# Kernel tuning notes

Hardware: AMD Instinct MI355X
Metric: run time of the kernel (lower is better)

Reference implementation:

```python
import jax, jax.numpy as jnp
import numpy as np

H = 1024   # hidden size
NH = 16    # num attention heads
HD = H // NH  # head dim = 64


def setup_inputs() -> dict:
    key = jax.random.key(0)
    ks = jax.random.split(key, 8)
    B, S = 2, 2048
    scale = 0.02
    return {
        "hidden_states": jax.random.normal(ks[0], (B, S, H), dtype=jnp.float32),
        "attention_mask": jnp.zeros((B, 1, 1, S), dtype=jnp.float32),
        "Wq": jax.random.normal(ks[1], (H, H), dtype=jnp.float32) * scale,
        "bq": jnp.zeros((H,), dtype=jnp.float32),
        "Wk": jax.random.normal(ks[2], (H, H), dtype=jnp.float32) * scale,
        "bk": jnp.zeros((H,), dtype=jnp.float32),
        "Wv": jax.random.normal(ks[3], (H, H), dtype=jnp.float32) * scale,
        "bv": jnp.zeros((H,), dtype=jnp.float32),
    }


def reference(hidden_states, attention_mask, Wq, bq, Wk, bk, Wv, bv):
    B, S, _ = hidden_states.shape

    def split_heads(x):  # [B,S,H] -> [B,NH,S,HD]
        return x.reshape(B, S, NH, HD).transpose(0, 2, 1, 3)

    q = split_heads(hidden_states @ Wq.T + bq)
    k = split_heads(hidden_states @ Wk.T + bk)
    v = split_heads(hidden_states @ Wv.T + bv)

    # raw attention scores [B,NH,S,S]
    scores = jnp.einsum("bhqd,bhkd->bhqk", q, k) / jnp.sqrt(jnp.float32(HD))
    scores = scores + attention_mask  # additive mask, broadcast [B,1,1,S]
    probs = jax.nn.softmax(scores, axis=-1)
    # dropout(p=0.1) is identity in eval mode

    ctx = jnp.einsum("bhqk,bhkd->bhqd", probs, v)  # [B,NH,S,HD]
    return ctx.transpose(0, 2, 1, 3).reshape(B, S, H)
```

## Files before the change

kernel.cpp:

```cpp
#include <hip/hip_runtime.h>
#include <hip/hip_bf16.h>
#include <math.h>

#define HSZ 1024
#define NHD 16
#define SEQ 2048
#define BSZ 2
#define MTOT (BSZ*SEQ)

typedef __attribute__((ext_vector_type(4)))  float  f32x4;
typedef __attribute__((ext_vector_type(8)))  __bf16 bf16x8;

#define LOG2E 1.4426950408889634f

#if __has_builtin(__builtin_amdgcn_exp2f)
#define EXP2(x) __builtin_amdgcn_exp2f(x)
#else
#define EXP2(x) exp2f(x)
#endif

__device__ __forceinline__ unsigned short f2bf(float x) {
    union { float f; unsigned u; } v; v.f = x;
    unsigned r = v.u + 0x7FFFu + ((v.u >> 16) & 1u);
    return (unsigned short)(r >> 16);
}
__device__ __forceinline__ float bf2f(unsigned short u) {
    union { unsigned u; float f; } v; v.u = ((unsigned)u) << 16; return v.f;
}
__device__ __forceinline__ unsigned cvtpk(float lo, float hi) {
    unsigned r;
    asm("v_cvt_pk_bf16_f32 %0, %1, %2" : "=v"(r) : "v"(lo), "v"(hi));
    return r;
}

__global__ __launch_bounds__(256) void cvt_all(
    const float* __restrict__ h,  unsigned short* __restrict__ hd,
    const float* __restrict__ w0, unsigned short* __restrict__ w0d,
    const float* __restrict__ w1, unsigned short* __restrict__ w1d,
    const float* __restrict__ w2, unsigned short* __restrict__ w2d,
    const float* __restrict__ mask, unsigned short* __restrict__ mexpb)
{
    const int bid = blockIdx.x;
    if (bid >= 3584) {
        const int o = ((bid - 3584) * 256 + threadIdx.x) * 8;
        float4 a = *(const float4*)(mask + o);
        float4 b = *(const float4*)(mask + o + 4);
        uint4 v;
        v.x = f2bf(EXP2(a.x * LOG2E)) | ((unsigned)f2bf(EXP2(a.y * LOG2E)) << 16);
        v.y = f2bf(EXP2(a.z * LOG2E)) | ((unsigned)f2bf(EXP2(a.w * LOG2E)) << 16);
        v.z = f2bf(EXP2(b.x * LOG2E)) | ((unsigned)f2bf(EXP2(b.y * LOG2E)) << 16);
        v.w = f2bf(EXP2(b.z * LOG2E)) | ((unsigned)f2bf(EXP2(b.w * LOG2E)) << 16);
        *(uint4*)(mexpb + o) = v;
        return;
    }
    const float* s; unsigned short* d; int i;
    if (bid < 2048)      { s = h;  d = hd;  i = bid; }
    else if (bid < 2560) { s = w0; d = w0d; i = bid - 2048; }
    else if (bid < 3072) { s = w1; d = w1d; i = bid - 2560; }
    else                 { s = w2; d = w2d; i = bid - 3072; }
    const int o = (i * 256 + threadIdx.x) * 8;
    float4 a = *(const float4*)(s + o);
    float4 b = *(const float4*)(s + o + 4);
    uint4 v;
    v.x = f2bf(a.x) | ((unsigned)f2bf(a.y) << 16);
    v.y = f2bf(a.z) | ((unsigned)f2bf(a.w) << 16);
    v.z = f2bf(b.x) | ((unsigned)f2bf(b.y) << 16);
    v.w = f2bf(b.z) | ((unsigned)f2bf(b.w) << 16);
    *(uint4*)(d + o) = v;
}

__global__ __launch_bounds__(256) void qkv_gemm(
    const unsigned short* __restrict__ hb,
    const unsigned short* __restrict__ wq,
    const unsigned short* __restrict__ wk,
    const unsigned short* __restrict__ wv,
    const float* __restrict__ bq, const float* __restrict__ bk,
    const float* __restrict__ bv, const unsigned short* __restrict__ mexpb,
    unsigned short* __restrict__ qo, char* __restrict__ ko,
    char* __restrict__ vo)
{
    __shared__ __align__(16) unsigned short As[128 * 32];
    __shared__ __align__(16) unsigned short Bs[128 * 32];

    const int t = threadIdx.x;
    const int w = t >> 6, l = t & 63, g = l >> 4, c = l & 15;
    const int bn = blockIdx.x, bm = blockIdx.y;
    const int which = bn >> 3;
    const int n0 = (bn & 7) << 7;
    const int m0 = bm << 7;
    const unsigned short* W = (which == 0) ? wq : (which == 1) ? wk : wv;
    const float* bb = (which == 0) ? bq : (which == 1) ? bk : bv;
    const float scale = (which == 0) ? 0.125f * LOG2E : 1.0f;
    const int wr = w >> 1, wc = w & 1;

    float mexpf[16];
    if (which == 2) {
        #pragma unroll
        for (int mi = 0; mi < 4; ++mi) {
            const int mrow = m0 + wr * 64 + mi * 16 + g * 4;
            const int bi = mrow >> 11, si = mrow & 2047;
            const unsigned short* mp = mexpb + bi * SEQ + si;
            uint2 mv = *(const uint2*)mp;
            mexpf[mi * 4 + 0] = bf2f((unsigned short)(mv.x & 0xFFFF));
            mexpf[mi * 4 + 1] = bf2f((unsigned short)(mv.x >> 16));
            mexpf[mi * 4 + 2] = bf2f((unsigned short)(mv.y & 0xFFFF));
            mexpf[mi * 4 + 3] = bf2f((unsigned short)(mv.y >> 16));
        }
    }

    f32x4 acc[4][4];
    #pragma unroll
    for (int mi = 0; mi < 4; ++mi)
        #pragma unroll
        for (int ni = 0; ni < 4; ++ni) acc[mi][ni] = {0.f, 0.f, 0.f, 0.f};

    for (int k0 = 0; k0 < HSZ; k0 += 32) {
        #pragma unroll
        for (int i2 = 0; i2 < 2; ++i2) {
            const int chunk = 2 * w + i2;
            const int row = (chunk << 4) + (l >> 2);
            const int sg = (l & 3) ^ ((row >> 1) & 3);
            const char* ga = (const char*)hb +
                (((size_t)(m0 + row) << 10) + k0) * 2 + sg * 16;
            const char* gb = (const char*)W +
                (((size_t)(n0 + row) << 10) + k0) * 2 + sg * 16;
            __builtin_amdgcn_global_load_lds(
                (const __attribute__((address_space(1))) unsigned*)ga,
                (__attribute__((address_space(3))) unsigned*)((char*)As + chunk * 1024),
                16, 0, 0);
            __builtin_amdgcn_global_load_lds(
                (const __attribute__((address_space(1))) unsigned*)gb,
                (__attribute__((address_space(3))) unsigned*)((char*)Bs + chunk * 1024),
                16, 0, 0);
        }
        __syncthreads();

        bf16x8 af[4], bfr[4];
        #pragma unroll
        for (int mi = 0; mi < 4; ++mi) {
            const int row = wr * 64 + mi * 16 + c;
            const int gg = g ^ ((row >> 1) & 3);
            af[mi] = *(const bf16x8*)((const char*)As + row * 64 + gg * 16);
        }
        #pragma unroll
        for (int ni = 0; ni < 4; ++ni) {
            const int row = wc * 64 + ni * 16 + c;
            const int gg = g ^ ((row >> 1) & 3);
            bfr[ni] = *(const bf16x8*)((const char*)Bs + row * 64 + gg * 16);
        }
        #pragma unroll
        for (int mi = 0; mi < 4; ++mi)
            #pragma unroll
            for (int ni = 0; ni < 4; ++ni)
                acc[mi][ni] = __builtin_amdgcn_mfma_f32_16x16x32_bf16(
                    af[mi], bfr[ni], acc[mi][ni], 0, 0, 0);
        __syncthreads();
    }

    #pragma unroll
    for (int ni = 0; ni < 4; ++ni) {
        const int ncol = n0 + wc * 64 + ni * 16 + c;
        const int hh = ncol >> 6, d = ncol & 63;
        const float bsc = bb[ncol] * scale;
        #pragma unroll
        for (int mi = 0; mi < 4; ++mi) {
            #pragma unroll
            for (int j = 0; j < 4; ++j) {
                const int mrow = m0 + wr * 64 + mi * 16 + g * 4 + j;
                const int bi = mrow >> 11, si = mrow & 2047;
                float vf = acc[mi][ni][j] * scale + bsc;
                if (which == 2) vf *= mexpf[mi * 4 + j];
                const unsigned short val = f2bf(vf);
                const size_t bhoff = (size_t)(bi * NHD + hh);
                if (which == 0) {
                    qo[((bhoff * SEQ + si) << 6) + d] = val;
                } else if (which == 1) {
                    char* p = ko + (bhoff << 18) + ((size_t)(si >> 6) << 13)
                            + ((si & 63) << 7) + (((d << 1)) ^ ((si & 7) << 4));
                    *(unsigned short*)p = val;
                } else {
                    char* p = vo + (bhoff << 18) + ((size_t)(si >> 6) << 13)
                            + (d << 7) + (((si & 63) << 1) ^ ((d & 7) << 4));
                    *(unsigned short*)p = val;
                }
            }
        }
    }
}

__global__ __launch_bounds__(256) void attn_mfma(
    const unsigned short* __restrict__ qb, const char* __restrict__ kb,
    const char* __restrict__ vb, const unsigned short* __restrict__ mexpb,
    float* __restrict__ out)
{
    __shared__ __align__(16) char Kt[2][8192];
    __shared__ __align__(16) char Vt[2][8192];
    __shared__ __align__(16) unsigned Pl[4][16][32];

    const int t = threadIdx.x;
    const int w = t >> 6, l = t & 63, g = l >> 4, c = l & 15;
    const int qt = blockIdx.x, h = blockIdx.y, b = blockIdx.z;
    const int bh = b * NHD + h;
    const int q0 = qt * 64 + w * 16;

    const unsigned short* qp = qb + ((size_t)bh * SEQ + q0) * 64;
    const char* kbase = kb + ((size_t)bh << 18);
    const char* vbase = vb + ((size_t)bh << 18);
    const unsigned short* mep = mexpb + b * SEQ;

    bf16x8 qf[2];
    #pragma unroll
    for (int p = 0; p < 2; ++p)
        qf[p] = *(const bf16x8*)(qp + c * 64 + p * 32 + g * 8);

    f32x4 o[4];
    #pragma unroll
    for (int tt = 0; tt < 4; ++tt) o[tt] = {0.f, 0.f, 0.f, 0.f};
    f32x4 lsumacc = {0.f, 0.f, 0.f, 0.f};

    auto STAGE = [&](int tile, int buf) {
        const char* kg = kbase + tile * 8192 + w * 2048 + l * 16;
        const char* vg = vbase + tile * 8192 + w * 2048 + l * 16;
        #pragma unroll
        for (int i = 0; i < 2; ++i) {
            __builtin_amdgcn_global_load_lds(
                (const __attribute__((address_space(1))) unsigned*)(kg + i * 1024),
                (__attribute__((address_space(3))) unsigned*)(&Kt[buf][w * 2048 + i * 1024]),
                16, 0, 0);
            __builtin_amdgcn_global_load_lds(
                (const __attribute__((address_space(1))) unsigned*)(vg + i * 1024),
                (__attribute__((address_space(3))) unsigned*)(&Vt[buf][w * 2048 + i * 1024]),
                16, 0, 0);
        }
    };

    STAGE(0, 0);
    __syncthreads();

    for (int kt = 0; kt < 32; ++kt) {
        const int cur = kt & 1;
        const int kv0 = kt * 64;
        if (kt < 31) STAGE(kt + 1, cur ^ 1);

        bf16x8 mf[2];
        #pragma unroll
        for (int blk = 0; blk < 2; ++blk)
            mf[blk] = *(const bf16x8*)(mep + kv0 + blk * 32 + g * 8);

        bf16x8 kfr[4][2];
        #pragma unroll
        for (int t2 = 0; t2 < 4; ++t2)
            #pragma unroll
            for (int p = 0; p < 2; ++p)
                kfr[t2][p] = *(const bf16x8*)(&Kt[cur][(t2 * 16 + c) * 128
                                 + ((p * 64 + g * 16) ^ ((c & 7) << 4))]);

        f32x4 s[4];
        #pragma unroll
        for (int t2 = 0; t2 < 4; ++t2) s[t2] = {0.f, 0.f, 0.f, 0.f};
        __builtin_amdgcn_s_setprio(1);
        #pragma unroll
        for (int t2 = 0; t2 < 4; ++t2) {
            s[t2] = __builtin_amdgcn_mfma_f32_16x16x32_bf16(kfr[t2][0], qf[0], s[t2], 0, 0, 0);
            s[t2] = __builtin_amdgcn_mfma_f32_16x16x32_bf16(kfr[t2][1], qf[1], s[t2], 0, 0, 0);
        }
        __builtin_amdgcn_s_setprio(0);

        #pragma unroll
        for (int t2 = 0; t2 < 4; ++t2) {
            s[t2][0] = EXP2(s[t2][0]); s[t2][1] = EXP2(s[t2][1]);
            s[t2][2] = EXP2(s[t2][2]); s[t2][3] = EXP2(s[t2][3]);
        }

        #pragma unroll
        for (int t2 = 0; t2 < 4; ++t2) {
            uint2 pr;
            pr.x = cvtpk(s[t2][0], s[t2][1]);
            pr.y = cvtpk(s[t2][2], s[t2][3]);
            *(uint2*)&Pl[w][c][(8 * t2 + 2 * g) ^ ((c & 7) << 2)] = pr;
        }

        bf16x8 pfr[2];
        #pragma unroll
        for (int blk = 0; blk < 2; ++blk)
            pfr[blk] = *(const bf16x8*)&Pl[w][c][(16 * blk + 4 * g) ^ ((c & 7) << 2)];
        __builtin_amdgcn_s_setprio(1);
        #pragma unroll
        for (int blk = 0; blk < 2; ++blk)
            lsumacc = __builtin_amdgcn_mfma_f32_16x16x32_bf16(mf[blk], pfr[blk], lsumacc, 0, 0, 0);
        #pragma unroll
        for (int tt = 0; tt < 4; ++tt) {
            #pragma unroll
            for (int blk = 0; blk < 2; ++blk) {
                const bf16x8 vfr = *(const bf16x8*)(&Vt[cur][(tt * 16 + c) * 128
                                     + ((blk * 64 + g * 16) ^ ((c & 7) << 4))]);
                o[tt] = __builtin_amdgcn_mfma_f32_16x16x32_bf16(vfr, pfr[blk], o[tt], 0, 0, 0);
            }
        }
        __builtin_amdgcn_s_setprio(0);

        __syncthreads();
    }

    const float linv = 1.f / lsumacc[0];

    #pragma unroll
    for (int tt = 0; tt < 4; ++tt) {
        const size_t rowb = ((size_t)(b * SEQ + q0 + c) << 10) + h * 64 + 16 * tt + 4 * g;
        out[rowb + 0] = o[tt][0] * linv;
        out[rowb + 1] = o[tt][1] * linv;
        out[rowb + 2] = o[tt][2] * linv;
        out[rowb + 3] = o[tt][3] * linv;
    }
}

extern "C" void kernel_launch(void* const* d_in, const int* in_sizes, int n_in,
                              void* d_out, int out_size, void* d_ws, size_t ws_size,
                              hipStream_t stream) {
    const float* hid  = (const float*)d_in[0];
    const float* mask = (const float*)d_in[1];
    const float* Wq   = (const float*)d_in[2];
    const float* bq   = (const float*)d_in[3];
    const float* Wk   = (const float*)d_in[4];
    const float* bk   = (const float*)d_in[5];
    const float* Wv   = (const float*)d_in[6];
    const float* bv   = (const float*)d_in[7];
    float* out = (float*)d_out;

    char* ws = (char*)d_ws;
    unsigned short* qbf = (unsigned short*)(ws);
    char*           kbf = ws + 8388608;
    char*           vbf = ws + 16777216;
    unsigned short* hbf = (unsigned short*)(ws + 25165824);
    unsigned short* wqb = (unsigned short*)(ws + 33554432);
    unsigned short* wkb = (unsigned short*)(ws + 35651584);
    unsigned short* wvb = (unsigned short*)(ws + 37748736);
    unsigned short* mxb = (unsigned short*)(ws + 39845888);

    cvt_all<<<3586, 256, 0, stream>>>(hid, hbf, Wq, wqb, Wk, wkb, Wv, wvb,
                                      mask, mxb);
    qkv_gemm<<<dim3(24, 32), 256, 0, stream>>>(hbf, wqb, wkb, wvb,
                                               bq, bk, bv, mxb, qbf, kbf, vbf);
    attn_mfma<<<dim3(32, NHD, BSZ), 256, 0, stream>>>(qbf, kbf, vbf, mxb, out);
}
```

Baseline: 120.3 us.

## Process two 16-row query tiles per wave to reuse K/V fragments

Each wave now handles 32 query rows (two 16-row sub-tiles), so each block covers 128 queries and the grid halves to 16 query tiles. K and V fragments read from LDS are reused across both sub-tiles, halving LDS reads and global K/V staging per query. The Pl scratch buffer is reused sequentially for the two sub-tiles. This raises register pressure (doubled accumulators and V fragments held live) and halves block count, which lowers occupancy and parallelism: 512 blocks on 256 CUs.

```diff
diff --git a/kernel.cpp b/kernel.cpp
--- a/kernel.cpp
+++ b/kernel.cpp
@@ -201,22 +201,24 @@
     const int w = t >> 6, l = t & 63, g = l >> 4, c = l & 15;
     const int qt = blockIdx.x, h = blockIdx.y, b = blockIdx.z;
     const int bh = b * NHD + h;
-    const int q0 = qt * 64 + w * 16;
+    const int q0 = qt * 128 + w * 32;
 
     const unsigned short* qp = qb + ((size_t)bh * SEQ + q0) * 64;
     const char* kbase = kb + ((size_t)bh << 18);
     const char* vbase = vb + ((size_t)bh << 18);
     const unsigned short* mep = mexpb + b * SEQ;
 
-    bf16x8 qf[2];
-    #pragma unroll
-    for (int p = 0; p < 2; ++p)
-        qf[p] = *(const bf16x8*)(qp + c * 64 + p * 32 + g * 8);
-
-    f32x4 o[4];
-    #pragma unroll
-    for (int tt = 0; tt < 4; ++tt) o[tt] = {0.f, 0.f, 0.f, 0.f};
-    f32x4 lsumacc = {0.f, 0.f, 0.f, 0.f};
+    bf16x8 qf[2][2];
+    #pragma unroll
+    for (int qh = 0; qh < 2; ++qh)
+        #pragma unroll
+        for (int p = 0; p < 2; ++p)
+            qf[qh][p] = *(const bf16x8*)(qp + (qh * 16 + c) * 64 + p * 32 + g * 8);
+
+    f32x4 o0[4], o1[4];
+    #pragma unroll
+    for (int tt = 0; tt < 4; ++tt) { o0[tt] = {0.f,0.f,0.f,0.f}; o1[tt] = {0.f,0.f,0.f,0.f}; }
+    f32x4 ls0 = {0.f,0.f,0.f,0.f}, ls1 = {0.f,0.f,0.f,0.f};
 
     auto STAGE = [&](int tile, int buf) {
         const char* kg = kbase + tile * 8192 + w * 2048 + l * 16;
@@ -247,70 +249,106 @@
         for (int blk = 0; blk < 2; ++blk)
             mf[blk] = *(const bf16x8*)(mep + kv0 + blk * 32 + g * 8);
 
-        bf16x8 kfr[4][2];
-        #pragma unroll
-        for (int t2 = 0; t2 < 4; ++t2)
-            #pragma unroll
-            for (int p = 0; p < 2; ++p)
-                kfr[t2][p] = *(const bf16x8*)(&Kt[cur][(t2 * 16 + c) * 128
-                                 + ((p * 64 + g * 16) ^ ((c & 7) << 4))]);
-
-        f32x4 s[4];
-        #pragma unroll
-        for (int t2 = 0; t2 < 4; ++t2) s[t2] = {0.f, 0.f, 0.f, 0.f};
+        f32x4 s0[4], s1[4];
+        #pragma unroll
+        for (int t2 = 0; t2 < 4; ++t2) { s0[t2] = {0.f,0.f,0.f,0.f}; s1[t2] = {0.f,0.f,0.f,0.f}; }
         __builtin_amdgcn_s_setprio(1);
         #pragma unroll
         for (int t2 = 0; t2 < 4; ++t2) {
-            s[t2] = __builtin_amdgcn_mfma_f32_16x16x32_bf16(kfr[t2][0], qf[0], s[t2], 0, 0, 0);
-            s[t2] = __builtin_amdgcn_mfma_f32_16x16x32_bf16(kfr[t2][1], qf[1], s[t2], 0, 0, 0);
+            const bf16x8 k0 = *(const bf16x8*)(&Kt[cur][(t2 * 16 + c) * 128
+                                 + ((g * 16) ^ ((c & 7) << 4))]);
+            const bf16x8 k1 = *(const bf16x8*)(&Kt[cur][(t2 * 16 + c) * 128
+                                 + ((64 + g * 16) ^ ((c & 7) << 4))]);
+            s0[t2] = __builtin_amdgcn_mfma_f32_16x16x32_bf16(k0, qf[0][0], s0[t2], 0, 0, 0);
+            s0[t2] = __builtin_amdgcn_mfma_f32_16x16x32_bf16(k1, qf[0][1], s0[t2], 0, 0, 0);
+            s1[t2] = __builtin_amdgcn_mfma_f32_16x16x32_bf16(k0, qf[1][0], s1[t2], 0, 0, 0);
+            s1[t2] = __builtin_amdgcn_mfma_f32_16x16x32_bf16(k1, qf[1][1], s1[t2], 0, 0, 0);
         }
         __builtin_amdgcn_s_setprio(0);
 
-        #pragma unroll
-        for (int t2 = 0; t2 < 4; ++t2) {
-            s[t2][0] = EXP2(s[t2][0]); s[t2][1] = EXP2(s[t2][1]);
-            s[t2][2] = EXP2(s[t2][2]); s[t2][3] = EXP2(s[t2][3]);
-        }
-
+        bf16x8 vfr[4][2];
+        #pragma unroll
+        for (int tt = 0; tt < 4; ++tt)
+            #pragma unroll
+            for (int blk = 0; blk < 2; ++blk)
+                vfr[tt][blk] = *(const bf16x8*)(&Vt[cur][(tt * 16 + c) * 128
+                                     + ((blk * 64 + g * 16) ^ ((c & 7) << 4))]);
+
+        #pragma unroll
+        for (int t2 = 0; t2 < 4; ++t2) {
+            s0[t2][0] = EXP2(s0[t2][0]); s0[t2][1] = EXP2(s0[t2][1]);
+            s0[t2][2] = EXP2(s0[t2][2]); s0[t2][3] = EXP2(s0[t2][3]);
+        }
         #pragma unroll
         for (int t2 = 0; t2 < 4; ++t2) {
             uint2 pr;
-            pr.x = cvtpk(s[t2][0], s[t2][1]);
-            pr.y = cvtpk(s[t2][2], s[t2][3]);
+            pr.x = cvtpk(s0[t2][0], s0[t2][1]);
+            pr.y = cvtpk(s0[t2][2], s0[t2][3]);
             *(uint2*)&Pl[w][c][(8 * t2 + 2 * g) ^ ((c & 7) << 2)] = pr;
         }
-
-        bf16x8 pfr[2];
-        #pragma unroll
-        for (int blk = 0; blk < 2; ++blk)
-            pfr[blk] = *(const bf16x8*)&Pl[w][c][(16 * blk + 4 * g) ^ ((c & 7) << 2)];
-        __builtin_amdgcn_s_setprio(1);
-        #pragma unroll
-        for (int blk = 0; blk < 2; ++blk)
-            lsumacc = __builtin_amdgcn_mfma_f32_16x16x32_bf16(mf[blk], pfr[blk], lsumacc, 0, 0, 0);
-        #pragma unroll
-        for (int tt = 0; tt < 4; ++tt) {
-            #pragma unroll
-            for (int blk = 0; blk < 2; ++blk) {
-                const bf16x8 vfr = *(const bf16x8*)(&Vt[cur][(tt * 16 + c) * 128
-                                     + ((blk * 64 + g * 16) ^ ((c & 7) << 4))]);
-                o[tt] = __builtin_amdgcn_mfma_f32_16x16x32_bf16(vfr, pfr[blk], o[tt], 0, 0, 0);
-            }
-        }
-        __builtin_amdgcn_s_setprio(0);
+        {
+            bf16x8 pfr[2];
+            #pragma unroll
+            for (int blk = 0; blk < 2; ++blk)
+                pfr[blk] = *(const bf16x8*)&Pl[w][c][(16 * blk + 4 * g) ^ ((c & 7) << 2)];
+            __builtin_amdgcn_s_setprio(1);
+            #pragma unroll
+            for (int blk = 0; blk < 2; ++blk)
+                ls0 = __builtin_amdgcn_mfma_f32_16x16x32_bf16(mf[blk], pfr[blk], ls0, 0, 0, 0);
+            #pragma unroll
+            for (int tt = 0; tt < 4; ++tt)
+                #pragma unroll
+                for (int blk = 0; blk < 2; ++blk)
+                    o0[tt] = __builtin_amdgcn_mfma_f32_16x16x32_bf16(vfr[tt][blk], pfr[blk], o0[tt], 0, 0, 0);
+            __builtin_amdgcn_s_setprio(0);
+        }
+
+        #pragma unroll
+        for (int t2 = 0; t2 < 4; ++t2) {
+            s1[t2][0] = EXP2(s1[t2][0]); s1[t2][1] = EXP2(s1[t2][1]);
+            s1[t2][2] = EXP2(s1[t2][2]); s1[t2][3] = EXP2(s1[t2][3]);
+        }
+        #pragma unroll
+        for (int t2 = 0; t2 < 4; ++t2) {
+            uint2 pr;
+            pr.x = cvtpk(s1[t2][0], s1[t2][1]);
+            pr.y = cvtpk(s1[t2][2], s1[t2][3]);
+            *(uint2*)&Pl[w][c][(8 * t2 + 2 * g) ^ ((c & 7) << 2)] = pr;
+        }
+        {
+            bf16x8 pfr[2];
+            #pragma unroll
+            for (int blk = 0; blk < 2; ++blk)
+                pfr[blk] = *(const bf16x8*)&Pl[w][c][(16 * blk + 4 * g) ^ ((c & 7) << 2)];
+            __builtin_amdgcn_s_setprio(1);
+            #pragma unroll
+            for (int blk = 0; blk < 2; ++blk)
+                ls1 = __builtin_amdgcn_mfma_f32_16x16x32_bf16(mf[blk], pfr[blk], ls1, 0, 0, 0);
+            #pragma unroll
+            for (int tt = 0; tt < 4; ++tt)
+                #pragma unroll
+                for (int blk = 0; blk < 2; ++blk)
+                    o1[tt] = __builtin_amdgcn_mfma_f32_16x16x32_bf16(vfr[tt][blk], pfr[blk], o1[tt], 0, 0, 0);
+            __builtin_amdgcn_s_setprio(0);
+        }
 
         __syncthreads();
     }
 
-    const float linv = 1.f / lsumacc[0];
-
+    const float li0 = 1.f / ls0[0];
+    const float li1 = 1.f / ls1[0];
     #pragma unroll
     for (int tt = 0; tt < 4; ++tt) {
-        const size_t rowb = ((size_t)(b * SEQ + q0 + c) << 10) + h * 64 + 16 * tt + 4 * g;
-        out[rowb + 0] = o[tt][0] * linv;
-        out[rowb + 1] = o[tt][1] * linv;
-        out[rowb + 2] = o[tt][2] * linv;
-        out[rowb + 3] = o[tt][3] * linv;
+        const size_t r0 = ((size_t)(b * SEQ + q0 + c) << 10) + h * 64 + 16 * tt + 4 * g;
+        out[r0 + 0] = o0[tt][0] * li0;
+        out[r0 + 1] = o0[tt][1] * li0;
+        out[r0 + 2] = o0[tt][2] * li0;
+        out[r0 + 3] = o0[tt][3] * li0;
+        const size_t r1 = ((size_t)(b * SEQ + q0 + 16 + c) << 10) + h * 64 + 16 * tt + 4 * g;
+        out[r1 + 0] = o1[tt][0] * li1;
+        out[r1 + 1] = o1[tt][1] * li1;
+        out[r1 + 2] = o1[tt][2] * li1;
+        out[r1 + 3] = o1[tt][3] * li1;
     }
 }
 
@@ -341,5 +379,5 @@
                                       mask, mxb);
     qkv_gemm<<<dim3(24, 32), 256, 0, stream>>>(hbf, wqb, wkb, wvb,
                                                bq, bk, bv, mxb, qbf, kbf, vbf);
-    attn_mfma<<<dim3(32, NHD, BSZ), 256, 0, stream>>>(qbf, kbf, vbf, mxb, out);
-}
+    attn_mfma<<<dim3(16, NHD, BSZ), 256, 0, stream>>>(qbf, kbf, vbf, mxb, out);
+}
```

Measured after the change: 118.4 us. Within noise of the previous version (-1.6%).
